# Kernel tuning notes

Measured on AMD Instinct MI355X. Metric: run time of the kernel, lower is better.

The kernel has to match this reference:

```python
import jax, jax.numpy as jnp
import numpy as np

B, L, D = 8, 4096, 768


def setup_inputs() -> dict:
    key = jax.random.key(0)
    k1, = jax.random.split(key, 1)
    x = jax.random.normal(k1, (B, L, D), dtype=jnp.float32)
    alpha = jnp.ones((L, 1), dtype=jnp.float32)  # nn.Parameter(torch.ones(l_dim, 1))
    return {"x": x, "alpha": alpha}


def reference(x, alpha):
    # Original: y = (x @ x^T).mean(-1, keepdim=True) / D
    # Algebraically identical (mean over j of sum_d x_i,d x_j,d = x_i . mean_j x_j):
    d = x.shape[-1]
    l = x.shape[1]
    mean_x = jnp.mean(x, axis=1)                       # [B, D]
    y = jnp.einsum('bld,bd->bl', x, mean_x)[..., None] / d  # [B, L, 1]
    # Original: y = (y @ y^T).mean(-1, keepdim=True) / L
    # (y y^T)_ij = y_i * y_j; mean over j = y_i * mean(y)
    y = y * jnp.mean(y, axis=1, keepdims=True) / l     # [B, L, 1]
    # y * x + alpha  (alpha broadcast over batch and D); dropout p=0 -> identity
    return alpha + y * x
```

## Files before the change

kernel.cpp:

```cpp
#include <hip/hip_runtime.h>

constexpr int Bn = 8;
constexpr int Ln = 4096;
constexpr int Dn = 768;
constexpr int CHUNKS = 64;
constexpr int RPC = Ln / CHUNKS;

__global__ void k_colsum_part(const float* __restrict__ x, float4* __restrict__ part) {
    int b = blockIdx.x / CHUNKS;
    int c = blockIdx.x % CHUNKS;
    int t = threadIdx.x;
    const float4* xb = (const float4*)(x + ((size_t)b * Ln + (size_t)c * RPC) * Dn);
    float4 s = {0.f, 0.f, 0.f, 0.f};
    for (int l = 0; l < RPC; ++l) {
        float4 v = xb[(size_t)l * (Dn / 4) + t];
        s.x += v.x; s.y += v.y; s.z += v.z; s.w += v.w;
    }
    part[((size_t)b * CHUNKS + c) * (Dn / 4) + t] = s;
}

__global__ void k_scale(const float* __restrict__ part, float* __restrict__ m) {
    int b = blockIdx.x;
    int t = threadIdx.x;
    const float* pb = part + (size_t)b * CHUNKS * Dn;
    float s0 = 0.f, s1 = 0.f, s2 = 0.f;
    for (int c = 0; c < CHUNKS; ++c) {
        const float* row = pb + (size_t)c * Dn;
        s0 += row[t];
        s1 += row[t + 256];
        s2 += row[t + 512];
    }
    float ssq = s0 * s0 + s1 * s1 + s2 * s2;
    #pragma unroll
    for (int off = 1; off < 64; off <<= 1) ssq += __shfl_xor(ssq, off);
    __shared__ float wsum[4];
    int wave = t >> 6, lane = t & 63;
    if (lane == 0) wsum[wave] = ssq;
    __syncthreads();
    float ss = wsum[0] + wsum[1] + wsum[2] + wsum[3];

    const float f1 = 1.0f / ((float)Ln * (float)Dn);
    float scale = ss * f1 * f1 / ((float)Ln * (float)Ln);
    m[b * Dn + t]       = s0 * scale;
    m[b * Dn + t + 256] = s1 * scale;
    m[b * Dn + t + 512] = s2 * scale;
}

__global__ void k_fused(const float* __restrict__ x, const float* __restrict__ m,
                        const float* __restrict__ alpha, float* __restrict__ out) {
    int wave = threadIdx.x >> 6;
    int lane = threadIdx.x & 63;
    int row  = blockIdx.x * 4 + wave;
    int b    = row >> 12;
    int l    = row & (Ln - 1);

    const float4* xr = (const float4*)(x + (size_t)row * Dn);
    const float4* mr = (const float4*)(m + (size_t)b * Dn);

    float4 x0 = xr[lane], x1 = xr[lane + 64], x2 = xr[lane + 128];
    float4 m0 = mr[lane], m1 = mr[lane + 64], m2 = mr[lane + 128];

    float acc = x0.x * m0.x + x0.y * m0.y + x0.z * m0.z + x0.w * m0.w
              + x1.x * m1.x + x1.y * m1.y + x1.z * m1.z + x1.w * m1.w
              + x2.x * m2.x + x2.y * m2.y + x2.z * m2.z + x2.w * m2.w;
    #pragma unroll
    for (int off = 1; off < 64; off <<= 1) acc += __shfl_xor(acc, off);

    float a = alpha[l];
    float4* orow = (float4*)(out + (size_t)row * Dn);
    float4 o0 = {a + acc * x0.x, a + acc * x0.y, a + acc * x0.z, a + acc * x0.w};
    float4 o1 = {a + acc * x1.x, a + acc * x1.y, a + acc * x1.z, a + acc * x1.w};
    float4 o2 = {a + acc * x2.x, a + acc * x2.y, a + acc * x2.z, a + acc * x2.w};
    orow[lane]       = o0;
    orow[lane + 64]  = o1;
    orow[lane + 128] = o2;
}

extern "C" void kernel_launch(void* const* d_in, const int* in_sizes, int n_in,
                              void* d_out, int out_size, void* d_ws, size_t ws_size,
                              hipStream_t stream) {
    const float* x     = (const float*)d_in[0];
    const float* alpha = (const float*)d_in[1];
    float* out = (float*)d_out;

    float* part = (float*)d_ws;
    float* m    = part + (size_t)Bn * CHUNKS * Dn;

    k_colsum_part<<<Bn * CHUNKS, 192, 0, stream>>>(x, (float4*)part);
    k_scale<<<Bn, 256, 0, stream>>>(part, m);
    k_fused<<<(Bn * Ln) / 4, 256, 0, stream>>>(x, m, alpha, out);
}
```

Baseline: 197.1 us.

## Fuse colsum, scale, and apply into one cooperative persistent kernel

Merges the three kernels into a single cooperative kernel separated by grid-wide syncs, with each block handling the same row chunks in the reduction and apply phases. This removes two kernel launches and may let the second read of x hit in cache. In exchange it adds grid.sync overhead and leaves most blocks idle during the small per-batch scale phase. It also limits the grid to the resident-occupancy size, which could reduce memory-level parallelism.

```diff
diff --git a/kernel.cpp b/kernel.cpp
--- a/kernel.cpp
+++ b/kernel.cpp
@@ -1,79 +1,108 @@
 #include <hip/hip_runtime.h>
+#include <hip/hip_cooperative_groups.h>
+
+namespace cg = cooperative_groups;
 
 constexpr int Bn = 8;
 constexpr int Ln = 4096;
 constexpr int Dn = 768;
-constexpr int CHUNKS = 64;
-constexpr int RPC = Ln / CHUNKS;
+constexpr int D4 = Dn / 4;
+constexpr int THREADS = 384;
+constexpr int CHUNKS_TOT = 512;
+constexpr int RPC = (Bn * Ln) / CHUNKS_TOT;
+constexpr int CPB = CHUNKS_TOT / Bn;
 
-__global__ void k_colsum_part(const float* __restrict__ x, float4* __restrict__ part) {
-    int b = blockIdx.x / CHUNKS;
-    int c = blockIdx.x % CHUNKS;
-    int t = threadIdx.x;
-    const float4* xb = (const float4*)(x + ((size_t)b * Ln + (size_t)c * RPC) * Dn);
-    float4 s = {0.f, 0.f, 0.f, 0.f};
-    for (int l = 0; l < RPC; ++l) {
-        float4 v = xb[(size_t)l * (Dn / 4) + t];
-        s.x += v.x; s.y += v.y; s.z += v.z; s.w += v.w;
+__global__ __launch_bounds__(THREADS, 3)
+void k_all(const float* __restrict__ x, const float* __restrict__ alpha,
+           float* __restrict__ out, float* __restrict__ part,
+           float* __restrict__ m) {
+    cg::grid_group grid = cg::this_grid();
+    const int t    = threadIdx.x;
+    const int h    = t / 192;
+    const int col  = t % 192;
+    __shared__ float4 buf[D4];
+    __shared__ float  wsum[3];
+
+    const float4* x4    = (const float4*)x;
+    float4*       part4 = (float4*)part;
+    float4*       m4    = (float4*)m;
+
+    for (int ch = blockIdx.x; ch < CHUNKS_TOT; ch += gridDim.x) {
+        const float4* p = x4 + ((size_t)ch * RPC + h * 32) * D4 + col;
+        float4 s = {0.f, 0.f, 0.f, 0.f};
+        #pragma unroll 4
+        for (int l = 0; l < 32; ++l) {
+            float4 v = p[(size_t)l * D4];
+            s.x += v.x; s.y += v.y; s.z += v.z; s.w += v.w;
+        }
+        __syncthreads();
+        if (h == 1) buf[col] = s;
+        __syncthreads();
+        if (h == 0) {
+            float4 o = buf[col];
+            s.x += o.x; s.y += o.y; s.z += o.z; s.w += o.w;
+            part4[(size_t)ch * D4 + col] = s;
+        }
     }
-    part[((size_t)b * CHUNKS + c) * (Dn / 4) + t] = s;
-}
 
-__global__ void k_scale(const float* __restrict__ part, float* __restrict__ m) {
-    int b = blockIdx.x;
-    int t = threadIdx.x;
-    const float* pb = part + (size_t)b * CHUNKS * Dn;
-    float s0 = 0.f, s1 = 0.f, s2 = 0.f;
-    for (int c = 0; c < CHUNKS; ++c) {
-        const float* row = pb + (size_t)c * Dn;
-        s0 += row[t];
-        s1 += row[t + 256];
-        s2 += row[t + 512];
+    grid.sync();
+
+    for (int b = blockIdx.x; b < Bn; b += gridDim.x) {
+        const float4* pb = part4 + (size_t)b * CPB * D4;
+        float4 s = {0.f, 0.f, 0.f, 0.f};
+        for (int c = h * 32; c < h * 32 + 32; ++c) {
+            float4 v = pb[(size_t)c * D4 + col];
+            s.x += v.x; s.y += v.y; s.z += v.z; s.w += v.w;
+        }
+        if (h == 1) buf[col] = s;
+        __syncthreads();
+        float4 cs = {0.f, 0.f, 0.f, 0.f};
+        if (h == 0) {
+            float4 o = buf[col];
+            cs.x = s.x + o.x; cs.y = s.y + o.y;
+            cs.z = s.z + o.z; cs.w = s.w + o.w;
+            float ssq = cs.x * cs.x + cs.y * cs.y + cs.z * cs.z + cs.w * cs.w;
+            #pragma unroll
+            for (int off = 1; off < 64; off <<= 1) ssq += __shfl_xor(ssq, off);
+            if ((t & 63) == 0) wsum[t >> 6] = ssq;
+        }
+        __syncthreads();
+        if (h == 0) {
+            float ss = wsum[0] + wsum[1] + wsum[2];
+            const float f1 = 1.0f / ((float)Ln * (float)Dn);
+            float scale = ss * f1 * f1 / ((float)Ln * (float)Ln);
+            float4 mv = {cs.x * scale, cs.y * scale, cs.z * scale, cs.w * scale};
+            m4[(size_t)b * D4 + col] = mv;
+        }
+        __syncthreads();
     }
-    float ssq = s0 * s0 + s1 * s1 + s2 * s2;
-    #pragma unroll
-    for (int off = 1; off < 64; off <<= 1) ssq += __shfl_xor(ssq, off);
-    __shared__ float wsum[4];
-    int wave = t >> 6, lane = t & 63;
-    if (lane == 0) wsum[wave] = ssq;
-    __syncthreads();
-    float ss = wsum[0] + wsum[1] + wsum[2] + wsum[3];
 
-    const float f1 = 1.0f / ((float)Ln * (float)Dn);
-    float scale = ss * f1 * f1 / ((float)Ln * (float)Ln);
-    m[b * Dn + t]       = s0 * scale;
-    m[b * Dn + t + 256] = s1 * scale;
-    m[b * Dn + t + 512] = s2 * scale;
-}
+    grid.sync();
 
-__global__ void k_fused(const float* __restrict__ x, const float* __restrict__ m,
-                        const float* __restrict__ alpha, float* __restrict__ out) {
-    int wave = threadIdx.x >> 6;
-    int lane = threadIdx.x & 63;
-    int row  = blockIdx.x * 4 + wave;
-    int b    = row >> 12;
-    int l    = row & (Ln - 1);
-
-    const float4* xr = (const float4*)(x + (size_t)row * Dn);
-    const float4* mr = (const float4*)(m + (size_t)b * Dn);
-
-    float4 x0 = xr[lane], x1 = xr[lane + 64], x2 = xr[lane + 128];
-    float4 m0 = mr[lane], m1 = mr[lane + 64], m2 = mr[lane + 128];
-
-    float acc = x0.x * m0.x + x0.y * m0.y + x0.z * m0.z + x0.w * m0.w
-              + x1.x * m1.x + x1.y * m1.y + x1.z * m1.z + x1.w * m1.w
-              + x2.x * m2.x + x2.y * m2.y + x2.z * m2.z + x2.w * m2.w;
-    #pragma unroll
-    for (int off = 1; off < 64; off <<= 1) acc += __shfl_xor(acc, off);
-
-    float a = alpha[l];
-    float4* orow = (float4*)(out + (size_t)row * Dn);
-    float4 o0 = {a + acc * x0.x, a + acc * x0.y, a + acc * x0.z, a + acc * x0.w};
-    float4 o1 = {a + acc * x1.x, a + acc * x1.y, a + acc * x1.z, a + acc * x1.w};
-    float4 o2 = {a + acc * x2.x, a + acc * x2.y, a + acc * x2.z, a + acc * x2.w};
-    orow[lane]       = o0;
-    orow[lane + 64]  = o1;
-    orow[lane + 128] = o2;
+    const int wave = t >> 6, lane = t & 63;
+    for (int ch = blockIdx.x; ch < CHUNKS_TOT; ch += gridDim.x) {
+        const int row0 = ch * RPC;
+        const float4* mr = m4 + (size_t)(row0 >> 12) * D4;
+        float4 m0 = mr[lane], m1 = mr[lane + 64], m2 = mr[lane + 128];
+        for (int r = wave; r < RPC; r += 6) {
+            const int row = row0 + r;
+            const float4* xr = x4 + (size_t)row * D4;
+            float4 x0 = xr[lane], x1 = xr[lane + 64], x2 = xr[lane + 128];
+            float acc = x0.x * m0.x + x0.y * m0.y + x0.z * m0.z + x0.w * m0.w
+                      + x1.x * m1.x + x1.y * m1.y + x1.z * m1.z + x1.w * m1.w
+                      + x2.x * m2.x + x2.y * m2.y + x2.z * m2.z + x2.w * m2.w;
+            #pragma unroll
+            for (int off = 1; off < 64; off <<= 1) acc += __shfl_xor(acc, off);
+            float a = alpha[row & (Ln - 1)];
+            float4* orow = (float4*)out + (size_t)row * D4;
+            float4 o0 = {a + acc * x0.x, a + acc * x0.y, a + acc * x0.z, a + acc * x0.w};
+            float4 o1 = {a + acc * x1.x, a + acc * x1.y, a + acc * x1.z, a + acc * x1.w};
+            float4 o2 = {a + acc * x2.x, a + acc * x2.y, a + acc * x2.z, a + acc * x2.w};
+            orow[lane]       = o0;
+            orow[lane + 64]  = o1;
+            orow[lane + 128] = o2;
+        }
+    }
 }
 
 extern "C" void kernel_launch(void* const* d_in, const int* in_sizes, int n_in,
@@ -81,12 +110,23 @@
                               hipStream_t stream) {
     const float* x     = (const float*)d_in[0];
     const float* alpha = (const float*)d_in[1];
-    float* out = (float*)d_out;
+    float* out  = (float*)d_out;
 
     float* part = (float*)d_ws;
-    float* m    = part + (size_t)Bn * CHUNKS * Dn;
+    float* m    = part + (size_t)CHUNKS_TOT * Dn;
 
-    k_colsum_part<<<Bn * CHUNKS, 192, 0, stream>>>(x, (float4*)part);
-    k_scale<<<Bn, 256, 0, stream>>>(part, m);
-    k_fused<<<(Bn * Ln) / 4, 256, 0, stream>>>(x, m, alpha, out);
+    static int grid = 0;
+    if (grid == 0) {
+        int occ = 0;
+        if (hipOccupancyMaxActiveBlocksPerMultiprocessor(
+                &occ, reinterpret_cast<const void*>(k_all), THREADS, 0) != hipSuccess ||
+            occ < 1)
+            occ = 1;
+        grid = occ * 256;
+        if (grid > CHUNKS_TOT) grid = CHUNKS_TOT;
+    }
+
+    void* args[] = {(void*)&x, (void*)&alpha, (void*)&out, (void*)&part, (void*)&m};
+    hipLaunchCooperativeKernel(reinterpret_cast<const void*>(k_all),
+                               dim3(grid), dim3(THREADS), args, 0u, stream);
 }
```

Result: slower. 320.3 us (+62.5%).

## Spread column-sum fold across more blocks and recompute scale per wave

Applied to the files above, without the earlier changes.

Doubles the number of column-sum chunks per batch and replaces the 8-block scale kernel with a 96-block fold kernel, which exposes more parallelism in the small middle stage. Each wave in the fused kernel now recomputes the sum-of-squares scale factor from the column sums with a wave reduction, so the separate scale pass goes away. Output stores become nontemporal to avoid polluting cache, and the first pass gets unrolling and launch bounds. The cost is redundant reduction work in every wave of the main kernel and a larger partials buffer.

```diff
diff --git a/kernel.cpp b/kernel.cpp
--- a/kernel.cpp
+++ b/kernel.cpp
@@ -3,77 +3,78 @@
 constexpr int Bn = 8;
 constexpr int Ln = 4096;
 constexpr int Dn = 768;
-constexpr int CHUNKS = 64;
-constexpr int RPC = Ln / CHUNKS;
+constexpr int D4 = Dn / 4;
+constexpr int CPB = 128;
+constexpr int CHUNKS_TOT = Bn * CPB;
+constexpr int RPC = Ln / CPB;
 
-__global__ void k_colsum_part(const float* __restrict__ x, float4* __restrict__ part) {
-    int b = blockIdx.x / CHUNKS;
-    int c = blockIdx.x % CHUNKS;
-    int t = threadIdx.x;
-    const float4* xb = (const float4*)(x + ((size_t)b * Ln + (size_t)c * RPC) * Dn);
+typedef float vfloat4 __attribute__((ext_vector_type(4)));
+
+__global__ __launch_bounds__(192)
+void k_colsum_part(const float4* __restrict__ x, float4* __restrict__ part) {
+    const int ch = blockIdx.x;
+    const int t  = threadIdx.x;
+    const float4* p = x + (size_t)ch * RPC * D4 + t;
     float4 s = {0.f, 0.f, 0.f, 0.f};
+    #pragma unroll 8
     for (int l = 0; l < RPC; ++l) {
-        float4 v = xb[(size_t)l * (Dn / 4) + t];
+        float4 v = p[(size_t)l * D4];
         s.x += v.x; s.y += v.y; s.z += v.z; s.w += v.w;
     }
-    part[((size_t)b * CHUNKS + c) * (Dn / 4) + t] = s;
+    part[(size_t)ch * D4 + t] = s;
 }
 
-__global__ void k_scale(const float* __restrict__ part, float* __restrict__ m) {
-    int b = blockIdx.x;
-    int t = threadIdx.x;
-    const float* pb = part + (size_t)b * CHUNKS * Dn;
-    float s0 = 0.f, s1 = 0.f, s2 = 0.f;
-    for (int c = 0; c < CHUNKS; ++c) {
-        const float* row = pb + (size_t)c * Dn;
-        s0 += row[t];
-        s1 += row[t + 256];
-        s2 += row[t + 512];
-    }
-    float ssq = s0 * s0 + s1 * s1 + s2 * s2;
+__global__ __launch_bounds__(64)
+void k_colsum_fold(const float* __restrict__ part, float* __restrict__ colsum) {
+    const int b    = blockIdx.x / 12;
+    const int sl   = blockIdx.x % 12;
+    const int lane = threadIdx.x;
+    const float* pb = part + (size_t)b * CPB * Dn + sl * 64 + lane;
+    float s = 0.f;
+    #pragma unroll 8
+    for (int c = 0; c < CPB; ++c) s += pb[(size_t)c * Dn];
+    colsum[b * Dn + sl * 64 + lane] = s;
+}
+
+__global__ __launch_bounds__(256)
+void k_fused(const float4* __restrict__ x, const float4* __restrict__ colsum,
+             const float* __restrict__ alpha, vfloat4* __restrict__ out) {
+    const int wave = threadIdx.x >> 6;
+    const int lane = threadIdx.x & 63;
+    const int row  = blockIdx.x * 4 + wave;
+    const int b    = row >> 12;
+    const int l    = row & (Ln - 1);
+
+    const float4* cs = colsum + (size_t)b * D4;
+    float4 c0 = cs[lane], c1 = cs[lane + 64], c2 = cs[lane + 128];
+
+    float ssq = c0.x * c0.x + c0.y * c0.y + c0.z * c0.z + c0.w * c0.w
+              + c1.x * c1.x + c1.y * c1.y + c1.z * c1.z + c1.w * c1.w
+              + c2.x * c2.x + c2.y * c2.y + c2.z * c2.z + c2.w * c2.w;
     #pragma unroll
     for (int off = 1; off < 64; off <<= 1) ssq += __shfl_xor(ssq, off);
-    __shared__ float wsum[4];
-    int wave = t >> 6, lane = t & 63;
-    if (lane == 0) wsum[wave] = ssq;
-    __syncthreads();
-    float ss = wsum[0] + wsum[1] + wsum[2] + wsum[3];
 
-    const float f1 = 1.0f / ((float)Ln * (float)Dn);
-    float scale = ss * f1 * f1 / ((float)Ln * (float)Ln);
-    m[b * Dn + t]       = s0 * scale;
-    m[b * Dn + t + 256] = s1 * scale;
-    m[b * Dn + t + 512] = s2 * scale;
-}
+    const float4* xr = x + (size_t)row * D4;
+    float4 x0 = xr[lane], x1 = xr[lane + 64], x2 = xr[lane + 128];
 
-__global__ void k_fused(const float* __restrict__ x, const float* __restrict__ m,
-                        const float* __restrict__ alpha, float* __restrict__ out) {
-    int wave = threadIdx.x >> 6;
-    int lane = threadIdx.x & 63;
-    int row  = blockIdx.x * 4 + wave;
-    int b    = row >> 12;
-    int l    = row & (Ln - 1);
-
-    const float4* xr = (const float4*)(x + (size_t)row * Dn);
-    const float4* mr = (const float4*)(m + (size_t)b * Dn);
-
-    float4 x0 = xr[lane], x1 = xr[lane + 64], x2 = xr[lane + 128];
-    float4 m0 = mr[lane], m1 = mr[lane + 64], m2 = mr[lane + 128];
-
-    float acc = x0.x * m0.x + x0.y * m0.y + x0.z * m0.z + x0.w * m0.w
-              + x1.x * m1.x + x1.y * m1.y + x1.z * m1.z + x1.w * m1.w
-              + x2.x * m2.x + x2.y * m2.y + x2.z * m2.z + x2.w * m2.w;
+    float acc = x0.x * c0.x + x0.y * c0.y + x0.z * c0.z + x0.w * c0.w
+              + x1.x * c1.x + x1.y * c1.y + x1.z * c1.z + x1.w * c1.w
+              + x2.x * c2.x + x2.y * c2.y + x2.z * c2.z + x2.w * c2.w;
     #pragma unroll
     for (int off = 1; off < 64; off <<= 1) acc += __shfl_xor(acc, off);
 
-    float a = alpha[l];
-    float4* orow = (float4*)(out + (size_t)row * Dn);
-    float4 o0 = {a + acc * x0.x, a + acc * x0.y, a + acc * x0.z, a + acc * x0.w};
-    float4 o1 = {a + acc * x1.x, a + acc * x1.y, a + acc * x1.z, a + acc * x1.w};
-    float4 o2 = {a + acc * x2.x, a + acc * x2.y, a + acc * x2.z, a + acc * x2.w};
-    orow[lane]       = o0;
-    orow[lane + 64]  = o1;
-    orow[lane + 128] = o2;
+    const float f1 = 1.0f / ((float)Ln * (float)Dn);
+    const float k  = ssq * f1 * f1 / ((float)Ln * (float)Ln);
+    const float coef = acc * k;
+
+    const float a = alpha[l];
+    vfloat4* orow = out + (size_t)row * D4;
+    vfloat4 o0 = {a + coef * x0.x, a + coef * x0.y, a + coef * x0.z, a + coef * x0.w};
+    vfloat4 o1 = {a + coef * x1.x, a + coef * x1.y, a + coef * x1.z, a + coef * x1.w};
+    vfloat4 o2 = {a + coef * x2.x, a + coef * x2.y, a + coef * x2.z, a + coef * x2.w};
+    __builtin_nontemporal_store(o0, &orow[lane]);
+    __builtin_nontemporal_store(o1, &orow[lane + 64]);
+    __builtin_nontemporal_store(o2, &orow[lane + 128]);
 }
 
 extern "C" void kernel_launch(void* const* d_in, const int* in_sizes, int n_in,
@@ -83,10 +84,11 @@
     const float* alpha = (const float*)d_in[1];
     float* out = (float*)d_out;
 
-    float* part = (float*)d_ws;
-    float* m    = part + (size_t)Bn * CHUNKS * Dn;
+    float* part   = (float*)d_ws;
+    float* colsum = part + (size_t)CHUNKS_TOT * Dn;
 
-    k_colsum_part<<<Bn * CHUNKS, 192, 0, stream>>>(x, (float4*)part);
-    k_scale<<<Bn, 256, 0, stream>>>(part, m);
-    k_fused<<<(Bn * Ln) / 4, 256, 0, stream>>>(x, m, alpha, out);
+    k_colsum_part<<<CHUNKS_TOT, 192, 0, stream>>>((const float4*)x, (float4*)part);
+    k_colsum_fold<<<Bn * 12, 64, 0, stream>>>(part, colsum);
+    k_fused<<<(Bn * Ln) / 4, 256, 0, stream>>>((const float4*)x, (const float4*)colsum,
+                                               alpha, (vfloat4*)out);
 }
```

Measured after the change: 196.4 us. About the same (-0.4%).
